# Kernel optimization log

Hardware: AMD Instinct MI355X
Metric: run time of the kernel (lower is better)

Reference implementation:

```python
import jax, jax.numpy as jnp
import numpy as np

B, S, D = 4, 1024, 512
H, HD, M = 8, 64, 2
EPS = 1e-5


def setup_inputs() -> dict:
    key = jax.random.key(0)
    ks = jax.random.split(key, 8)
    scale = 0.02
    x = jax.random.normal(ks[0], (B, S, D), dtype=jnp.float32)
    Wq = jax.random.normal(ks[1], (D, D), dtype=jnp.float32) * scale
    Wk = jax.random.normal(ks[2], (D, D), dtype=jnp.float32) * scale
    Wv = jax.random.normal(ks[3], (D, D), dtype=jnp.float32) * scale
    Wo = jax.random.normal(ks[4], (D, D), dtype=jnp.float32) * scale
    bo = jnp.zeros((D,), dtype=jnp.float32)
    Wg = jax.random.normal(ks[5], (H * (2 + M), D), dtype=jnp.float32) * scale
    bg = jnp.zeros((H * (2 + M),), dtype=jnp.float32)
    init_decays = jnp.array([0.95, 0.8], dtype=jnp.float32)
    logit = jnp.log(init_decays / (1.0 - init_decays))
    logit_alphas = jnp.tile(logit[None, :], (H, 1))  # [H, M]
    ln_w = jnp.ones((D,), dtype=jnp.float32)
    ln_b = jnp.zeros((D,), dtype=jnp.float32)
    return {"x": x, "Wq": Wq, "Wk": Wk, "Wv": Wv, "Wo": Wo, "bo": bo,
            "Wg": Wg, "bg": bg, "logit_alphas": logit_alphas,
            "ln_w": ln_w, "ln_b": ln_b}


def _rope(x):
    # x: [B, S, H, HD] interleaved rotary
    half = HD // 2
    inv_freq = 1.0 / (10000.0 ** (jnp.arange(half, dtype=jnp.float32) / half))
    t = jnp.arange(S, dtype=jnp.float32)
    freqs = t[:, None] * inv_freq[None, :]            # [S, half]
    cos = jnp.cos(freqs)[None, :, None, :]            # [1, S, 1, half]
    sin = jnp.sin(freqs)[None, :, None, :]
    x1, x2 = x[..., ::2], x[..., 1::2]
    o1 = x1 * cos - x2 * sin
    o2 = x1 * sin + x2 * cos
    return jnp.stack((o1, o2), axis=-1).reshape(x.shape)


def _forward(x, Wq, Wk, Wv, Wo, bo, Wg, bg, logit_alphas, ln_w, ln_b):
    residual = x
    q = (x @ Wq.T).reshape(B, S, H, HD)
    k = (x @ Wk.T).reshape(B, S, H, HD)
    v = (x @ Wv.T).reshape(B, S, H, HD)
    q = _rope(q)
    k = _rope(k)

    gates = (x @ Wg.T + bg).reshape(B, S, H, 2 + M)
    g_f = jax.nn.sigmoid(gates[..., 0])               # [B, S, H]
    g_u = jax.nn.sigmoid(gates[..., 1])               # [B, S, H]
    w_mix = jax.nn.softmax(gates[..., 2:], axis=-1)   # [B, S, H, M]
    alphas = jax.nn.sigmoid(logit_alphas)             # [H, M]

    # time-major for scan
    qs = jnp.moveaxis(q, 1, 0)       # [S, B, H, HD]
    ks = jnp.moveaxis(k, 1, 0)
    vs = jnp.moveaxis(v, 1, 0)
    gfs = jnp.moveaxis(g_f, 1, 0)    # [S, B, H]
    gus = jnp.moveaxis(g_u, 1, 0)
    wms = jnp.moveaxis(w_mix, 1, 0)  # [S, B, H, M]

    state0 = jnp.zeros((B, H, M, HD, HD), dtype=x.dtype)

    def step(state, inp):
        qt, kt, vt, gf, gu, wt = inp
        retain = alphas[None, :, :] * gf[:, :, None]           # [B, H, M]
        write_w = wt * gu[..., None]                           # [B, H, M]
        outer = jnp.einsum('bhd,bhe->bhde', kt, vt)            # [B, H, HD, HD]
        state = (state * retain[..., None, None]
                 + outer[:, :, None, :, :] * write_w[..., None, None])
        S_read = jnp.einsum('bhmde,bhm->bhde', state, wt)      # [B, H, HD, HD]
        o = jnp.einsum('bhd,bhde->bhe', qt, S_read)            # [B, H, HD]
        return state, o

    _, outs = jax.lax.scan(step, state0, (qs, ks, vs, gfs, gus, wms))
    out = jnp.moveaxis(outs, 0, 1).reshape(B, S, H * HD)
    out = out @ Wo.T + bo
    y = residual + out
    mu = jnp.mean(y, axis=-1, keepdims=True)
    var = jnp.mean(jnp.square(y - mu), axis=-1, keepdims=True)
    return (y - mu) / jnp.sqrt(var + EPS) * ln_w + ln_b


def reference(x, Wq, Wk, Wv, Wo, bo, Wg, bg, logit_alphas, ln_w, ln_b):
    return _forward(x, Wq, Wk, Wv, Wo, bo, Wg, bg, logit_alphas, ln_w, ln_b)
```

## Files before the change

### kernel.cpp

```cpp
#include <hip/hip_runtime.h>
#include <hip/hip_bf16.h>
#include <math.h>

#define B_  4
#define S_  1024
#define D_  512
#define H_  8
#define HD_ 64
#define EPS_ 1e-5f

typedef __attribute__((ext_vector_type(8))) short  bf16x8;
typedef __attribute__((ext_vector_type(4))) short  bf16x4;
typedef __attribute__((ext_vector_type(4))) float  f32x4;

#define MFMA16(a, b, c) __builtin_amdgcn_mfma_f32_16x16x32_bf16((a), (b), (c), 0, 0, 0)

#define GLOAD16(gp, lp) __builtin_amdgcn_global_load_lds( \
    (const __attribute__((address_space(1))) unsigned int*)(gp), \
    (__attribute__((address_space(3))) unsigned int*)(lp), 16, 0, 0)

__device__ __forceinline__ float bf2f(short u) {
    union { unsigned int i; float f; } v;
    v.i = ((unsigned int)(unsigned short)u) << 16;
    return v.f;
}
__device__ __forceinline__ short f2bf(float f) {
    __hip_bfloat16 h = __float2bfloat16(f);
    return *reinterpret_cast<short*>(&h);
}

__global__ __launch_bounds__(256) void convert_inputs(
    const float* __restrict__ x,
    const float* __restrict__ Wq, const float* __restrict__ Wk,
    const float* __restrict__ Wv, const float* __restrict__ Wg,
    const float* __restrict__ Wo,
    short* __restrict__ xbf, short* __restrict__ Wcat, short* __restrict__ Wobf,
    float2* __restrict__ rope)
{
    const int id = blockIdx.x * 256 + threadIdx.x;
    if (id < 262144) {
        const size_t e = (size_t)id * 8;
        float4 v0 = *(const float4*)(x + e);
        float4 v1 = *(const float4*)(x + e + 4);
        bf16x8 o = { f2bf(v0.x), f2bf(v0.y), f2bf(v0.z), f2bf(v0.w),
                     f2bf(v1.x), f2bf(v1.y), f2bf(v1.z), f2bf(v1.w) };
        *(bf16x8*)(xbf + e) = o;
    } else if (id < 368640) {
        const int i2 = id - 262144;
        const int row = i2 >> 6;
        const int c8 = (i2 & 63) * 8;
        const float* s = nullptr;
        if (row < 512)       s = Wq + (size_t)row * 512 + c8;
        else if (row < 1024) s = Wk + (size_t)(row - 512) * 512 + c8;
        else if (row < 1536) s = Wv + (size_t)(row - 1024) * 512 + c8;
        else if (row < 1568) s = Wg + (size_t)(row - 1536) * 512 + c8;
        bf16x8 o = (bf16x8)0;
        if (s) {
            float4 v0 = *(const float4*)(s);
            float4 v1 = *(const float4*)(s + 4);
            o = bf16x8{ f2bf(v0.x), f2bf(v0.y), f2bf(v0.z), f2bf(v0.w),
                        f2bf(v1.x), f2bf(v1.y), f2bf(v1.z), f2bf(v1.w) };
        }
        *(bf16x8*)(Wcat + (size_t)row * 512 + c8) = o;
    } else if (id < 401408) {
        const int i3 = id - 368640;
        const size_t e = (size_t)i3 * 8;
        float4 v0 = *(const float4*)(Wo + e);
        float4 v1 = *(const float4*)(Wo + e + 4);
        bf16x8 o = { f2bf(v0.x), f2bf(v0.y), f2bf(v0.z), f2bf(v0.w),
                     f2bf(v1.x), f2bf(v1.y), f2bf(v1.z), f2bf(v1.w) };
        *(bf16x8*)(Wobf + e) = o;
    } else {
        const int i4 = id - 401408;
        const int s = i4 >> 5, i = i4 & 31;
        const float inv = exp2f(-(float)i * (13.287712379549449f / 32.0f));
        float sn, cs;
        sincosf((float)s * inv, &sn, &cs);
        rope[i4] = make_float2(cs, sn);
    }
}

__global__ __launch_bounds__(256) void mfma_proj(
    const short* __restrict__ Abf, const short* __restrict__ Wcat,
    const float2* __restrict__ rope,
    short* __restrict__ Qbf, short* __restrict__ Kbf,
    short* __restrict__ Vbf, float* __restrict__ Graw)
{
    __shared__ __align__(16) short lds[17408];
    short* sA = lds;
    short* sB = lds + 8192;

    const int p = blockIdx.x;
    const int xcd = p & 7, slot = p >> 3;
    const int by = xcd + 8 * (slot / 13);
    const int bx = slot % 13;
    const int n0 = bx * 128, m0 = by * 128;

    const int tid = threadIdx.x;
    const int lane = tid & 63, wave = tid >> 6;
    const int lrow = lane & 15, lgrp = lane >> 4;
    const int wr = wave >> 1, wc = wave & 1;
    const int srl = lane >> 3;
    const int scs = (lane & 7) * 8;

    f32x4 acc[4][4];
    #pragma unroll
    for (int i = 0; i < 4; ++i)
        #pragma unroll
        for (int j = 0; j < 4; ++j) acc[i][j] = (f32x4)0.f;

    for (int step = 0; step < 8; ++step) {
        const int kt = step * 64;
        #pragma unroll
        for (int i = 0; i < 4; ++i) {
            const int chunk = i * 4 + wave;
            const int r = chunk * 8 + srl;
            GLOAD16(Abf  + (size_t)(m0 + r) * 512 + kt + scs, sA + chunk * 512);
            GLOAD16(Wcat + (size_t)(n0 + r) * 512 + kt + scs, sB + chunk * 512);
        }
        __syncthreads();
        #pragma unroll
        for (int kk = 0; kk < 2; ++kk) {
            const int kb = kk * 32 + lgrp * 8;
            bf16x8 af[4], bfr[4];
            #pragma unroll
            for (int mi = 0; mi < 4; ++mi)
                af[mi] = *(const bf16x8*)&sA[(wr * 64 + mi * 16 + lrow) * 64 + kb];
            #pragma unroll
            for (int ni = 0; ni < 4; ++ni)
                bfr[ni] = *(const bf16x8*)&sB[(wc * 64 + ni * 16 + lrow) * 64 + kb];
            #pragma unroll
            for (int mi = 0; mi < 4; ++mi)
                #pragma unroll
                for (int ni = 0; ni < 4; ++ni)
                    acc[mi][ni] = MFMA16(af[mi], bfr[ni], acc[mi][ni]);
        }
        __syncthreads();
    }

    if (n0 < 1536) {
        short* stg = lds;
        #pragma unroll
        for (int mi = 0; mi < 4; ++mi)
            #pragma unroll
            for (int ni = 0; ni < 4; ++ni)
                #pragma unroll
                for (int j = 0; j < 4; ++j) {
                    const int rl = wr * 64 + mi * 16 + lgrp * 4 + j;
                    const int cl = wc * 64 + ni * 16 + lrow;
                    stg[rl * 136 + cl] = f2bf(acc[mi][ni][j]);
                }
        __syncthreads();
        short* dst; int dstoff; bool roped;
        if (n0 < 512)       { dst = Qbf; dstoff = n0;        roped = true;  }
        else if (n0 < 1024) { dst = Kbf; dstoff = n0 - 512;  roped = true;  }
        else                { dst = Vbf; dstoff = n0 - 1024; roped = false; }
        #pragma unroll
        for (int it = 0; it < 8; ++it) {
            const int c8 = tid + it * 256;
            const int row = c8 >> 4, co = (c8 & 15) * 8;
            bf16x8 vv = *(const bf16x8*)&stg[row * 136 + co];
            if (roped) {
                const int s = (m0 + row) & (S_ - 1);
                const int ib = ((dstoff + co) & 63) >> 1;
                #pragma unroll
                for (int j = 0; j < 4; ++j) {
                    const float2 t = rope[s * 32 + ib + j];
                    const float xr = bf2f(vv[2 * j]), xi = bf2f(vv[2 * j + 1]);
                    vv[2 * j]     = f2bf(xr * t.x - xi * t.y);
                    vv[2 * j + 1] = f2bf(xr * t.y + xi * t.x);
                }
            }
            *(bf16x8*)(dst + (size_t)(m0 + row) * 512 + dstoff + co) = vv;
        }
    } else {
        #pragma unroll
        for (int mi = 0; mi < 4; ++mi)
            #pragma unroll
            for (int ni = 0; ni < 2; ++ni) {
                const int col = wc * 64 + ni * 16 + lrow;
                if (col < 32) {
                    #pragma unroll
                    for (int j = 0; j < 4; ++j) {
                        const int row = m0 + wr * 64 + mi * 16 + lgrp * 4 + j;
                        Graw[(size_t)row * 32 + col] = acc[mi][ni][j];
                    }
                }
            }
    }
}

__global__ __launch_bounds__(256) void chunk_delta(
    const short* __restrict__ Kbf, const short* __restrict__ Vbf,
    const float* __restrict__ Graw, const float* __restrict__ bg,
    const float* __restrict__ logit_alphas,
    short* __restrict__ Ubuf, float* __restrict__ SRb)
{
    __shared__ __align__(16) short sK [64 * 72];
    __shared__ __align__(16) short sVT[64 * 72];
    __shared__ __align__(16) short sKscT[2][64 * 72];
    __shared__ float sScal[64][4];
    __shared__ float sKs[2][64];

    const int tid  = threadIdx.x;
    const int wave = tid >> 6, lane = tid & 63;
    const int lrow = lane & 15, lgrp = lane >> 4;
    const int c  = blockIdx.x & 15;
    const int bh = blockIdx.x >> 4;
    const int h = bh & 7, b = bh >> 3;
    const int row0 = wave * 16;
    const int s0 = c * 64;

    if (tid < 64) {
        const int bs = b * S_ + s0 + tid;
        const float4 gv = *(const float4*)(Graw + (size_t)bs * 32 + h * 4);
        const float g0 = gv.x + bg[h * 4 + 0];
        const float g1 = gv.y + bg[h * 4 + 1];
        const float g2 = gv.z + bg[h * 4 + 2];
        const float g3 = gv.w + bg[h * 4 + 3];
        const float gf  = 1.f / (1.f + expf(-g0));
        const float gu  = 1.f / (1.f + expf(-g1));
        const float wm0 = 1.f / (1.f + expf(-(g2 - g3)));
        const float a0 = 1.f / (1.f + expf(-logit_alphas[h * 2 + 0]));
        const float a1 = 1.f / (1.f + expf(-logit_alphas[h * 2 + 1]));
        sScal[tid][0] = a0 * gf; sScal[tid][1] = a1 * gf;
        sScal[tid][2] = wm0 * gu; sScal[tid][3] = (1.f - wm0) * gu;
    }

    #pragma unroll
    for (int it = 0; it < 2; ++it) {
        const int i = tid + it * 256;
        const int r = i >> 3, c8 = (i & 7) * 8;
        const size_t g = ((size_t)(b * S_ + s0 + r)) * 512 + h * 64 + c8;
        bf16x8 k8 = *(const bf16x8*)(Kbf + g);
        bf16x8 v8 = *(const bf16x8*)(Vbf + g);
        *(bf16x8*)&sK[r * 72 + c8] = k8;
        #pragma unroll
        for (int j = 0; j < 8; ++j) sVT[(c8 + j) * 72 + r] = v8[j];
    }
    __syncthreads();

    if (wave < 2) {
        const int m = wave;
        float pre = log2f(sScal[lane][m]);
        #pragma unroll
        for (int off = 1; off < 64; off <<= 1) {
            const float u = __shfl_up(pre, off);
            if (lane >= off) pre += u;
        }
        const float lR = __shfl(pre, 63);
        sKs[m][lane] = sScal[lane][2 + m] * exp2f(lR - pre);
        if (lane == 63) SRb[blockIdx.x * 2 + m] = exp2f(lR);
    }
    __syncthreads();

    {
        const int task = tid >> 1, halfd = tid & 1;
        const int m = task >> 6, tau = task & 63;
        const float ksc = sKs[m][tau];
        #pragma unroll
        for (int dd = halfd * 32; dd < halfd * 32 + 32; dd += 8) {
            bf16x8 kr = *(const bf16x8*)&sK[tau * 72 + dd];
            #pragma unroll
            for (int j = 0; j < 8; ++j)
                sKscT[m][(dd + j) * 72 + tau] = f2bf(bf2f(kr[j]) * ksc);
        }
    }
    __syncthreads();

    #pragma unroll
    for (int m = 0; m < 2; ++m) {
        f32x4 accU[4];
        #pragma unroll
        for (int db = 0; db < 4; ++db) accU[db] = (f32x4)0.f;
        #pragma unroll
        for (int kk = 0; kk < 2; ++kk) {
            const int kb = kk * 32 + lgrp * 8;
            bf16x8 a = *(const bf16x8*)&sVT[(row0 + lrow) * 72 + kb];
            #pragma unroll
            for (int db = 0; db < 4; ++db) {
                bf16x8 bb = *(const bf16x8*)&sKscT[m][(db * 16 + lrow) * 72 + kb];
                accU[db] = MFMA16(a, bb, accU[db]);
            }
        }
        __syncthreads();
        #pragma unroll
        for (int db = 0; db < 4; ++db)
            #pragma unroll
            for (int r = 0; r < 4; ++r) {
                const int e = row0 + lgrp * 4 + r;
                sK[e * 72 + db * 16 + lrow] = f2bf(accU[db][r]);
            }
        __syncthreads();
        short* ub = Ubuf + ((size_t)blockIdx.x * 2 + m) * 4096;
        #pragma unroll
        for (int it = 0; it < 2; ++it) {
            const int i = tid + it * 256;
            const int e = i >> 3, seg = (i & 7) * 8;
            *(bf16x8*)(ub + e * 64 + seg) = *(const bf16x8*)&sK[e * 72 + seg];
        }
    }
}

__global__ __launch_bounds__(256) void state_prefix(
    short* __restrict__ Ubuf, const float* __restrict__ SRb)
{
    const int idx = blockIdx.x * 256 + threadIdx.x;
    const int ed2 = idx & 2047;
    const int m   = (idx >> 11) & 1;
    const int bh  = idx >> 12;
    float s0 = 0.f, s1 = 0.f;
    #pragma unroll
    for (int c = 0; c < 16; ++c) {
        const int bhc = bh * 16 + c;
        short* p = Ubuf + ((size_t)bhc * 2 + m) * 4096 + ed2 * 2;
        const float R = SRb[bhc * 2 + m];
        const short2 u = *(const short2*)p;
        const float u0 = bf2f(u.x), u1 = bf2f(u.y);
        *(short2*)p = make_short2(f2bf(s0), f2bf(s1));
        s0 = R * s0 + u0;
        s1 = R * s1 + u1;
    }
}

__global__ __launch_bounds__(256) void chunk_o(
    const short* __restrict__ Qbf, const short* __restrict__ Kbf,
    const short* __restrict__ Vbf, const float* __restrict__ Graw,
    const float* __restrict__ bg, const float* __restrict__ logit_alphas,
    const short* __restrict__ Ubuf, short* __restrict__ Obf)
{
    __shared__ __align__(16) short sQ [64 * 72];
    __shared__ __align__(16) short sK [64 * 72];
    __shared__ __align__(16) short sVT[64 * 72];
    __shared__ __align__(16) short sP [64 * 72];
    __shared__ __align__(16) short sST[2][64 * 72];
    __shared__ float sScal[64][6];
    __shared__ float sLc[2][64];
    __shared__ float sQs[2][64];

    const int tid  = threadIdx.x;
    const int wave = tid >> 6, lane = tid & 63;
    const int lrow = lane & 15, lgrp = lane >> 4;
    const int c  = blockIdx.x & 15;
    const int bh = blockIdx.x >> 4;
    const int h = bh & 7, b = bh >> 3;
    const int row0 = wave * 16;
    const int s0 = c * 64;

    if (tid < 64) {
        const int bs = b * S_ + s0 + tid;
        const float4 gv = *(const float4*)(Graw + (size_t)bs * 32 + h * 4);
        const float g0 = gv.x + bg[h * 4 + 0];
        const float g1 = gv.y + bg[h * 4 + 1];
        const float g2 = gv.z + bg[h * 4 + 2];
        const float g3 = gv.w + bg[h * 4 + 3];
        const float gf  = 1.f / (1.f + expf(-g0));
        const float gu  = 1.f / (1.f + expf(-g1));
        const float wm0 = 1.f / (1.f + expf(-(g2 - g3)));
        const float a0 = 1.f / (1.f + expf(-logit_alphas[h * 2 + 0]));
        const float a1 = 1.f / (1.f + expf(-logit_alphas[h * 2 + 1]));
        sScal[tid][0] = a0 * gf; sScal[tid][1] = a1 * gf;
        sScal[tid][2] = wm0 * gu; sScal[tid][3] = (1.f - wm0) * gu;
        sScal[tid][4] = wm0; sScal[tid][5] = 1.f - wm0;
    }

    #pragma unroll
    for (int it = 0; it < 2; ++it) {
        const int i = tid + it * 256;
        const int r = i >> 3, c8 = (i & 7) * 8;
        const size_t g = ((size_t)(b * S_ + s0 + r)) * 512 + h * 64 + c8;
        *(bf16x8*)&sQ[r * 72 + c8] = *(const bf16x8*)(Qbf + g);
        *(bf16x8*)&sK[r * 72 + c8] = *(const bf16x8*)(Kbf + g);
        bf16x8 v8 = *(const bf16x8*)(Vbf + g);
        #pragma unroll
        for (int j = 0; j < 8; ++j) sVT[(c8 + j) * 72 + r] = v8[j];
    }
    #pragma unroll
    for (int it = 0; it < 4; ++it) {
        const int c8 = tid + it * 256;
        const int m = c8 >> 9, rem = c8 & 511;
        const int e = rem >> 3, d8 = (rem & 7) * 8;
        *(bf16x8*)&sST[m][e * 72 + d8] =
            *(const bf16x8*)(Ubuf + ((size_t)blockIdx.x * 2 + m) * 4096 + e * 64 + d8);
    }
    __syncthreads();

    if (wave < 2) {
        const int m = wave;
        float pre = log2f(sScal[lane][m]);
        #pragma unroll
        for (int off = 1; off < 64; off <<= 1) {
            const float u = __shfl_up(pre, off);
            if (lane >= off) pre += u;
        }
        sLc[m][lane] = pre;
        sQs[m][lane] = sScal[lane][4 + m] * exp2f(pre);
    }
    __syncthreads();

    f32x4 accS[4], accO[4];
    #pragma unroll
    for (int cb = 0; cb < 4; ++cb) { accS[cb] = (f32x4)0.f; accO[cb] = (f32x4)0.f; }
    #pragma unroll
    for (int kk = 0; kk < 2; ++kk) {
        const int kb = kk * 32 + lgrp * 8;
        bf16x8 a = *(const bf16x8*)&sQ[(row0 + lrow) * 72 + kb];
        #pragma unroll
        for (int cb = 0; cb < 4; ++cb) {
            bf16x8 bb = *(const bf16x8*)&sK[(cb * 16 + lrow) * 72 + kb];
            accS[cb] = MFMA16(a, bb, accS[cb]);
        }
    }

    #pragma unroll
    for (int kk = 0; kk < 4; ++kk) {
        const int k0 = kk * 32 + lgrp * 8;
        const int m = k0 >> 6, d0 = k0 & 63;
        const float qs = sQs[m][row0 + lrow];
        bf16x8 qr = *(const bf16x8*)&sQ[(row0 + lrow) * 72 + d0];
        bf16x8 a;
        #pragma unroll
        for (int j = 0; j < 8; ++j) a[j] = f2bf(bf2f(qr[j]) * qs);
        #pragma unroll
        for (int cb = 0; cb < 4; ++cb) {
            bf16x8 bb = *(const bf16x8*)&sST[m][(cb * 16 + lrow) * 72 + d0];
            accO[cb] = MFMA16(a, bb, accO[cb]);
        }
    }

    #pragma unroll
    for (int r = 0; r < 4; ++r) {
        const int t = row0 + lgrp * 4 + r;
        const float wm0 = sScal[t][4], wm1 = sScal[t][5];
        const float lc0t = sLc[0][t],  lc1t = sLc[1][t];
        #pragma unroll
        for (int cb = 0; cb < 4; ++cb) {
            const int tau = cb * 16 + lrow;
            float p = 0.f;
            if (tau <= t) {
                const float c0 = wm0 * sScal[tau][2] * exp2f(lc0t - sLc[0][tau]);
                const float c1 = wm1 * sScal[tau][3] * exp2f(lc1t - sLc[1][tau]);
                p = accS[cb][r] * (c0 + c1);
            }
            sP[t * 72 + tau] = f2bf(p);
        }
    }

    #pragma unroll
    for (int kk = 0; kk < 2; ++kk) {
        const int kb = kk * 32 + lgrp * 8;
        bf16x8 a = *(const bf16x8*)&sP[(row0 + lrow) * 72 + kb];
        #pragma unroll
        for (int cb = 0; cb < 4; ++cb) {
            bf16x8 bb = *(const bf16x8*)&sVT[(cb * 16 + lrow) * 72 + kb];
            accO[cb] = MFMA16(a, bb, accO[cb]);
        }
    }

    #pragma unroll
    for (int cb = 0; cb < 4; ++cb)
        #pragma unroll
        for (int r = 0; r < 4; ++r) {
            const int t = row0 + lgrp * 4 + r;
            sP[t * 72 + cb * 16 + lrow] = f2bf(accO[cb][r]);
        }
    __syncthreads();
    #pragma unroll
    for (int it = 0; it < 2; ++it) {
        const int i = tid + it * 256;
        const int t = i >> 3, seg = (i & 7) * 8;
        *(bf16x8*)(Obf + ((size_t)(b * S_ + s0 + t)) * 512 + h * 64 + seg) =
            *(const bf16x8*)&sP[t * 72 + seg];
    }
}

__global__ __launch_bounds__(256) void mfma_out(
    const short* __restrict__ Abf, const short* __restrict__ Wobf,
    const float* __restrict__ bo, const float* __restrict__ xres,
    short* __restrict__ Ybf)
{
    __shared__ __align__(16) short lds[17408];
    short* sA = lds;
    short* sB = lds + 8192;

    const int p = blockIdx.x;
    const int xcd = p & 7, slot = p >> 3;
    const int by = xcd + 8 * (slot >> 2);
    const int bx = slot & 3;
    const int n0 = bx * 128, m0 = by * 128;

    const int tid = threadIdx.x;
    const int lane = tid & 63, wave = tid >> 6;
    const int lrow = lane & 15, lgrp = lane >> 4;
    const int wr = wave >> 1, wc = wave & 1;
    const int srl = lane >> 3;
    const int scs = (lane & 7) * 8;

    f32x4 acc[4][4];
    #pragma unroll
    for (int i = 0; i < 4; ++i)
        #pragma unroll
        for (int j = 0; j < 4; ++j) acc[i][j] = (f32x4)0.f;

    for (int step = 0; step < 8; ++step) {
        const int kt = step * 64;
        #pragma unroll
        for (int i = 0; i < 4; ++i) {
            const int chunk = i * 4 + wave;
            const int r = chunk * 8 + srl;
            GLOAD16(Abf  + (size_t)(m0 + r) * 512 + kt + scs, sA + chunk * 512);
            GLOAD16(Wobf + (size_t)(n0 + r) * 512 + kt + scs, sB + chunk * 512);
        }
        __syncthreads();
        #pragma unroll
        for (int kk = 0; kk < 2; ++kk) {
            const int kb = kk * 32 + lgrp * 8;
            bf16x8 af[4], bfr[4];
            #pragma unroll
            for (int mi = 0; mi < 4; ++mi)
                af[mi] = *(const bf16x8*)&sA[(wr * 64 + mi * 16 + lrow) * 64 + kb];
            #pragma unroll
            for (int ni = 0; ni < 4; ++ni)
                bfr[ni] = *(const bf16x8*)&sB[(wc * 64 + ni * 16 + lrow) * 64 + kb];
            #pragma unroll
            for (int mi = 0; mi < 4; ++mi)
                #pragma unroll
                for (int ni = 0; ni < 4; ++ni)
                    acc[mi][ni] = MFMA16(af[mi], bfr[ni], acc[mi][ni]);
        }
        __syncthreads();
    }

    short* stg = lds;
    #pragma unroll
    for (int mi = 0; mi < 4; ++mi)
        #pragma unroll
        for (int ni = 0; ni < 4; ++ni)
            #pragma unroll
            for (int j = 0; j < 4; ++j) {
                const int rl = wr * 64 + mi * 16 + lgrp * 4 + j;
                const int cl = wc * 64 + ni * 16 + lrow;
                stg[rl * 136 + cl] = f2bf(acc[mi][ni][j]);
            }
    __syncthreads();
    #pragma unroll
    for (int it = 0; it < 8; ++it) {
        const int c8 = tid + it * 256;
        const int row = c8 >> 4, co = (c8 & 15) * 8;
        const size_t gbase = (size_t)(m0 + row) * 512 + n0 + co;
        bf16x8 a = *(const bf16x8*)&stg[row * 136 + co];
        float4 x0 = *(const float4*)(xres + gbase);
        float4 x1 = *(const float4*)(xres + gbase + 4);
        float4 b0 = *(const float4*)(bo + n0 + co);
        float4 b1 = *(const float4*)(bo + n0 + co + 4);
        bf16x8 y;
        y[0] = f2bf(bf2f(a[0]) + b0.x + x0.x);
        y[1] = f2bf(bf2f(a[1]) + b0.y + x0.y);
        y[2] = f2bf(bf2f(a[2]) + b0.z + x0.z);
        y[3] = f2bf(bf2f(a[3]) + b0.w + x0.w);
        y[4] = f2bf(bf2f(a[4]) + b1.x + x1.x);
        y[5] = f2bf(bf2f(a[5]) + b1.y + x1.y);
        y[6] = f2bf(bf2f(a[6]) + b1.z + x1.z);
        y[7] = f2bf(bf2f(a[7]) + b1.w + x1.w);
        *(bf16x8*)(Ybf + gbase) = y;
    }
}

__global__ __launch_bounds__(256) void ln_kernel(
    const short* __restrict__ Ybf, const float* __restrict__ ln_w,
    const float* __restrict__ ln_b, float* __restrict__ out)
{
    const int wave = threadIdx.x >> 6;
    const int lane = threadIdx.x & 63;
    const int row = blockIdx.x * 4 + wave;

    bf16x8 v8 = *(const bf16x8*)(Ybf + (size_t)row * 512 + lane * 8);
    float v[8];
    #pragma unroll
    for (int j = 0; j < 8; ++j) v[j] = bf2f(v8[j]);

    float s = 0.f, sq = 0.f;
    #pragma unroll
    for (int j = 0; j < 8; ++j) { s += v[j]; sq += v[j] * v[j]; }
    #pragma unroll
    for (int off = 32; off; off >>= 1) {
        s  += __shfl_xor(s,  off);
        sq += __shfl_xor(sq, off);
    }
    const float mu  = s * (1.f / 512.f);
    const float var = sq * (1.f / 512.f) - mu * mu;
    const float inv = rsqrtf(var + EPS_);

    float4 w0 = *(const float4*)(ln_w + lane * 8);
    float4 w1 = *(const float4*)(ln_w + lane * 8 + 4);
    float4 b0 = *(const float4*)(ln_b + lane * 8);
    float4 b1 = *(const float4*)(ln_b + lane * 8 + 4);
    float4 o0, o1;
    o0.x = (v[0] - mu) * inv * w0.x + b0.x;
    o0.y = (v[1] - mu) * inv * w0.y + b0.y;
    o0.z = (v[2] - mu) * inv * w0.z + b0.z;
    o0.w = (v[3] - mu) * inv * w0.w + b0.w;
    o1.x = (v[4] - mu) * inv * w1.x + b1.x;
    o1.y = (v[5] - mu) * inv * w1.y + b1.y;
    o1.z = (v[6] - mu) * inv * w1.z + b1.z;
    o1.w = (v[7] - mu) * inv * w1.w + b1.w;
    *(float4*)(out + (size_t)row * 512 + lane * 8)     = o0;
    *(float4*)(out + (size_t)row * 512 + lane * 8 + 4) = o1;
}

extern "C" void kernel_launch(void* const* d_in, const int* in_sizes, int n_in,
                              void* d_out, int out_size, void* d_ws, size_t ws_size,
                              hipStream_t stream)
{
    const float* x   = (const float*)d_in[0];
    const float* Wq  = (const float*)d_in[1];
    const float* Wk  = (const float*)d_in[2];
    const float* Wv  = (const float*)d_in[3];
    const float* Wo  = (const float*)d_in[4];
    const float* bo  = (const float*)d_in[5];
    const float* Wg  = (const float*)d_in[6];
    const float* bg  = (const float*)d_in[7];
    const float* la  = (const float*)d_in[8];
    const float* lnw = (const float*)d_in[9];
    const float* lnb = (const float*)d_in[10];

    const size_t NQ = (size_t)B_ * S_ * D_;
    float* Graw = (float*)d_ws;
    float* ROPE = Graw + 131072;
    float* SRb  = ROPE + 65536;
    short* xbf  = (short*)(SRb + 1024);
    short* Wcat = xbf + NQ;
    short* Wobf = Wcat + (size_t)1664 * 512;
    short* Qbf  = Wobf + (size_t)512 * 512;
    short* Kbf  = Qbf + NQ;
    short* Vbf  = Kbf + NQ;
    short* Obf  = Vbf + NQ;
    short* Ybf  = Obf + NQ;
    short* Ubuf = Ybf + NQ;

    convert_inputs<<<1696, 256, 0, stream>>>(x, Wq, Wk, Wv, Wg, Wo, xbf, Wcat, Wobf,
                                             (float2*)ROPE);
    mfma_proj<<<416, 256, 0, stream>>>(xbf, Wcat, (const float2*)ROPE,
                                       Qbf, Kbf, Vbf, Graw);
    chunk_delta<<<512, 256, 0, stream>>>(Kbf, Vbf, Graw, bg, la, Ubuf, SRb);
    state_prefix<<<512, 256, 0, stream>>>(Ubuf, SRb);
    chunk_o<<<512, 256, 0, stream>>>(Qbf, Kbf, Vbf, Graw, bg, la, Ubuf, Obf);
    mfma_out<<<128, 256, 0, stream>>>(Obf, Wobf, bo, x, Ybf);
    ln_kernel<<<1024, 256, 0, stream>>>(Ybf, lnw, lnb, (float*)d_out);
}
```

Before: 135.1 us.

## Double-buffer GEMM tiles, fold state prefix into chunk_o, shrink out-proj tiles

Both MFMA GEMM kernels now double-buffer their LDS tiles, issuing the next k-step's global-to-LDS loads before computing on the current one, so load latency can overlap with MFMA work. The separate state_prefix kernel is removed. Each chunk_o block now recomputes its inter-chunk state prefix by walking over all earlier chunks' deltas, which saves a launch and a global round trip but adds redundant reads that grow with chunk index. The output projection uses 128x64 tiles over 256 blocks instead of 128x128 over 128, to fill more CUs.

Result: faster. 131.1 us (-2.9%).

```diff
diff --git a/kernel.cpp b/kernel.cpp
--- a/kernel.cpp
+++ b/kernel.cpp
@@ -86,9 +86,7 @@
     short* __restrict__ Qbf, short* __restrict__ Kbf,
     short* __restrict__ Vbf, float* __restrict__ Graw)
 {
-    __shared__ __align__(16) short lds[17408];
-    short* sA = lds;
-    short* sB = lds + 8192;
+    __shared__ __align__(16) short lds[32768];
 
     const int p = blockIdx.x;
     const int xcd = p & 7, slot = p >> 3;
@@ -109,16 +107,24 @@
         #pragma unroll
         for (int j = 0; j < 4; ++j) acc[i][j] = (f32x4)0.f;
 
+    #define PROJ_STAGE(buf, kt)  {                                            \
+        short* dA = lds + (buf) * 16384;                                      \
+        short* dB = dA + 8192;                                                \
+        _Pragma("unroll")                                                     \
+        for (int i = 0; i < 4; ++i) {                                         \
+            const int chunk = i * 4 + wave;                                   \
+            const int r = chunk * 8 + srl;                                    \
+            GLOAD16(Abf  + (size_t)(m0 + r) * 512 + (kt) + scs, dA + chunk * 512); \
+            GLOAD16(Wcat + (size_t)(n0 + r) * 512 + (kt) + scs, dB + chunk * 512); \
+        } }
+
+    PROJ_STAGE(0, 0);
+    __syncthreads();
+    int cur = 0;
     for (int step = 0; step < 8; ++step) {
-        const int kt = step * 64;
-        #pragma unroll
-        for (int i = 0; i < 4; ++i) {
-            const int chunk = i * 4 + wave;
-            const int r = chunk * 8 + srl;
-            GLOAD16(Abf  + (size_t)(m0 + r) * 512 + kt + scs, sA + chunk * 512);
-            GLOAD16(Wcat + (size_t)(n0 + r) * 512 + kt + scs, sB + chunk * 512);
-        }
-        __syncthreads();
+        if (step < 7) PROJ_STAGE(cur ^ 1, (step + 1) * 64);
+        const short* sA = lds + cur * 16384;
+        const short* sB = sA + 8192;
         #pragma unroll
         for (int kk = 0; kk < 2; ++kk) {
             const int kb = kk * 32 + lgrp * 8;
@@ -136,7 +142,9 @@
                     acc[mi][ni] = MFMA16(af[mi], bfr[ni], acc[mi][ni]);
         }
         __syncthreads();
-    }
+        cur ^= 1;
+    }
+    #undef PROJ_STAGE
 
     if (n0 < 1536) {
         short* stg = lds;
@@ -302,32 +310,12 @@
     }
 }
 
-__global__ __launch_bounds__(256) void state_prefix(
-    short* __restrict__ Ubuf, const float* __restrict__ SRb)
-{
-    const int idx = blockIdx.x * 256 + threadIdx.x;
-    const int ed2 = idx & 2047;
-    const int m   = (idx >> 11) & 1;
-    const int bh  = idx >> 12;
-    float s0 = 0.f, s1 = 0.f;
-    #pragma unroll
-    for (int c = 0; c < 16; ++c) {
-        const int bhc = bh * 16 + c;
-        short* p = Ubuf + ((size_t)bhc * 2 + m) * 4096 + ed2 * 2;
-        const float R = SRb[bhc * 2 + m];
-        const short2 u = *(const short2*)p;
-        const float u0 = bf2f(u.x), u1 = bf2f(u.y);
-        *(short2*)p = make_short2(f2bf(s0), f2bf(s1));
-        s0 = R * s0 + u0;
-        s1 = R * s1 + u1;
-    }
-}
-
 __global__ __launch_bounds__(256) void chunk_o(
     const short* __restrict__ Qbf, const short* __restrict__ Kbf,
     const short* __restrict__ Vbf, const float* __restrict__ Graw,
     const float* __restrict__ bg, const float* __restrict__ logit_alphas,
-    const short* __restrict__ Ubuf, short* __restrict__ Obf)
+    const short* __restrict__ Ubuf, const float* __restrict__ SRb,
+    short* __restrict__ Obf)
 {
     __shared__ __align__(16) short sQ [64 * 72];
     __shared__ __align__(16) short sK [64 * 72];
@@ -364,6 +352,34 @@
         sScal[tid][4] = wm0; sScal[tid][5] = 1.f - wm0;
     }
 
+    float sp[4][8];
+    #pragma unroll
+    for (int g = 0; g < 4; ++g)
+        #pragma unroll
+        for (int j = 0; j < 8; ++j) sp[g][j] = 0.f;
+    for (int cp = 0; cp < c; ++cp) {
+        const int bhc = bh * 16 + cp;
+        const float R0 = SRb[bhc * 2 + 0];
+        const float R1 = SRb[bhc * 2 + 1];
+        const short* ub = Ubuf + (size_t)bhc * 8192;
+        #pragma unroll
+        for (int g = 0; g < 4; ++g) {
+            bf16x8 u = *(const bf16x8*)(ub + g * 2048 + tid * 8);
+            const float R = (g < 2) ? R0 : R1;
+            #pragma unroll
+            for (int j = 0; j < 8; ++j) sp[g][j] = fmaf(R, sp[g][j], bf2f(u[j]));
+        }
+    }
+    #pragma unroll
+    for (int g = 0; g < 4; ++g) {
+        const int i = g * 2048 + tid * 8;
+        const int m = i >> 12, e = (i >> 6) & 63, d = i & 63;
+        bf16x8 o;
+        #pragma unroll
+        for (int j = 0; j < 8; ++j) o[j] = f2bf(sp[g][j]);
+        *(bf16x8*)&sST[m][e * 72 + d] = o;
+    }
+
     #pragma unroll
     for (int it = 0; it < 2; ++it) {
         const int i = tid + it * 256;
@@ -374,14 +390,6 @@
         bf16x8 v8 = *(const bf16x8*)(Vbf + g);
         #pragma unroll
         for (int j = 0; j < 8; ++j) sVT[(c8 + j) * 72 + r] = v8[j];
-    }
-    #pragma unroll
-    for (int it = 0; it < 4; ++it) {
-        const int c8 = tid + it * 256;
-        const int m = c8 >> 9, rem = c8 & 511;
-        const int e = rem >> 3, d8 = (rem & 7) * 8;
-        *(bf16x8*)&sST[m][e * 72 + d8] =
-            *(const bf16x8*)(Ubuf + ((size_t)blockIdx.x * 2 + m) * 4096 + e * 64 + d8);
     }
     __syncthreads();
 
@@ -479,15 +487,13 @@
     const float* __restrict__ bo, const float* __restrict__ xres,
     short* __restrict__ Ybf)
 {
-    __shared__ __align__(16) short lds[17408];
-    short* sA = lds;
-    short* sB = lds + 8192;
+    __shared__ __align__(16) short lds[24576];
 
     const int p = blockIdx.x;
     const int xcd = p & 7, slot = p >> 3;
-    const int by = xcd + 8 * (slot >> 2);
-    const int bx = slot & 3;
-    const int n0 = bx * 128, m0 = by * 128;
+    const int by = xcd + 8 * (slot >> 3);
+    const int bx = slot & 7;
+    const int n0 = bx * 64, m0 = by * 128;
 
     const int tid = threadIdx.x;
     const int lane = tid & 63, wave = tid >> 6;
@@ -496,63 +502,78 @@
     const int srl = lane >> 3;
     const int scs = (lane & 7) * 8;
 
-    f32x4 acc[4][4];
+    f32x4 acc[4][2];
     #pragma unroll
     for (int i = 0; i < 4; ++i)
         #pragma unroll
-        for (int j = 0; j < 4; ++j) acc[i][j] = (f32x4)0.f;
-
+        for (int j = 0; j < 2; ++j) acc[i][j] = (f32x4)0.f;
+
+    #define OUT_STAGE(buf, kt)  {                                             \
+        short* dA = lds + (buf) * 12288;                                      \
+        short* dB = dA + 8192;                                                \
+        _Pragma("unroll")                                                     \
+        for (int i = 0; i < 4; ++i) {                                         \
+            const int chunk = i * 4 + wave;                                   \
+            const int r = chunk * 8 + srl;                                    \
+            GLOAD16(Abf + (size_t)(m0 + r) * 512 + (kt) + scs, dA + chunk * 512); \
+        }                                                                     \
+        _Pragma("unroll")                                                     \
+        for (int i = 0; i < 2; ++i) {                                         \
+            const int chunk = i * 4 + wave;                                   \
+            const int r = chunk * 8 + srl;                                    \
+            GLOAD16(Wobf + (size_t)(n0 + r) * 512 + (kt) + scs, dB + chunk * 512); \
+        } }
+
+    OUT_STAGE(0, 0);
+    __syncthreads();
+    int cur = 0;
     for (int step = 0; step < 8; ++step) {
-        const int kt = step * 64;
-        #pragma unroll
-        for (int i = 0; i < 4; ++i) {
-            const int chunk = i * 4 + wave;
-            const int r = chunk * 8 + srl;
-            GLOAD16(Abf  + (size_t)(m0 + r) * 512 + kt + scs, sA + chunk * 512);
-            GLOAD16(Wobf + (size_t)(n0 + r) * 512 + kt + scs, sB + chunk * 512);
-        }
-        __syncthreads();
+        if (step < 7) OUT_STAGE(cur ^ 1, (step + 1) * 64);
+        const short* sA = lds + cur * 12288;
+        const short* sB = sA + 8192;
         #pragma unroll
         for (int kk = 0; kk < 2; ++kk) {
             const int kb = kk * 32 + lgrp * 8;
-            bf16x8 af[4], bfr[4];
+            bf16x8 af[4], bfr[2];
             #pragma unroll
             for (int mi = 0; mi < 4; ++mi)
                 af[mi] = *(const bf16x8*)&sA[(wr * 64 + mi * 16 + lrow) * 64 + kb];
             #pragma unroll
-            for (int ni = 0; ni < 4; ++ni)
-                bfr[ni] = *(const bf16x8*)&sB[(wc * 64 + ni * 16 + lrow) * 64 + kb];
+            for (int ni = 0; ni < 2; ++ni)
+                bfr[ni] = *(const bf16x8*)&sB[(wc * 32 + ni * 16 + lrow) * 64 + kb];
             #pragma unroll
             for (int mi = 0; mi < 4; ++mi)
                 #pragma unroll
-                for (int ni = 0; ni < 4; ++ni)
+                for (int ni = 0; ni < 2; ++ni)
                     acc[mi][ni] = MFMA16(af[mi], bfr[ni], acc[mi][ni]);
         }
         __syncthreads();
-    }
+        cur ^= 1;
+    }
+    #undef OUT_STAGE
 
     short* stg = lds;
     #pragma unroll
     for (int mi = 0; mi < 4; ++mi)
         #pragma unroll
-        for (int ni = 0; ni < 4; ++ni)
+        for (int ni = 0; ni < 2; ++ni)
             #pragma unroll
             for (int j = 0; j < 4; ++j) {
                 const int rl = wr * 64 + mi * 16 + lgrp * 4 + j;
-                const int cl = wc * 64 + ni * 16 + lrow;
-                stg[rl * 136 + cl] = f2bf(acc[mi][ni][j]);
+                const int cl = wc * 32 + ni * 16 + lrow;
+                stg[rl * 80 + cl] = f2bf(acc[mi][ni][j]);
             }
     __syncthreads();
     #pragma unroll
-    for (int it = 0; it < 8; ++it) {
-        const int c8 = tid + it * 256;
-        const int row = c8 >> 4, co = (c8 & 15) * 8;
-        const size_t gbase = (size_t)(m0 + row) * 512 + n0 + co;
-        bf16x8 a = *(const bf16x8*)&stg[row * 136 + co];
+    for (int it = 0; it < 4; ++it) {
+        const int u = tid + it * 256;
+        const int row = u >> 3, seg = (u & 7) * 8;
+        const size_t gbase = (size_t)(m0 + row) * 512 + n0 + seg;
+        bf16x8 a = *(const bf16x8*)&stg[row * 80 + seg];
         float4 x0 = *(const float4*)(xres + gbase);
         float4 x1 = *(const float4*)(xres + gbase + 4);
-        float4 b0 = *(const float4*)(bo + n0 + co);
-        float4 b1 = *(const float4*)(bo + n0 + co + 4);
+        float4 b0 = *(const float4*)(bo + n0 + seg);
+        float4 b1 = *(const float4*)(bo + n0 + seg + 4);
         bf16x8 y;
         y[0] = f2bf(bf2f(a[0]) + b0.x + x0.x);
         y[1] = f2bf(bf2f(a[1]) + b0.y + x0.y);
@@ -643,8 +664,7 @@
     mfma_proj<<<416, 256, 0, stream>>>(xbf, Wcat, (const float2*)ROPE,
                                        Qbf, Kbf, Vbf, Graw);
     chunk_delta<<<512, 256, 0, stream>>>(Kbf, Vbf, Graw, bg, la, Ubuf, SRb);
-    state_prefix<<<512, 256, 0, stream>>>(Ubuf, SRb);
-    chunk_o<<<512, 256, 0, stream>>>(Qbf, Kbf, Vbf, Graw, bg, la, Ubuf, Obf);
-    mfma_out<<<128, 256, 0, stream>>>(Obf, Wobf, bo, x, Ybf);
+    chunk_o<<<512, 256, 0, stream>>>(Qbf, Kbf, Vbf, Graw, bg, la, Ubuf, SRb, Obf);
+    mfma_out<<<256, 256, 0, stream>>>(Obf, Wobf, bo, x, Ybf);
     ln_kernel<<<1024, 256, 0, stream>>>(Ybf, lnw, lnb, (float*)d_out);
 }
```
